# Optimization experiments

Measured on AMD Instinct MI355X. Metric: run time of the kernel, lower is better.

The kernel has to match this reference:

```python
import jax, jax.numpy as jnp
import numpy as np

B, M, D, H, K, V = 4, 2048, 1024, 16, 64, 64

def setup_inputs() -> dict:
    key = jax.random.key(0)
    ks = jax.random.split(key, 5)
    return {
        "x": jax.random.normal(ks[0], (B, M, D), dtype=jnp.float32),
        "P_q": jax.random.normal(ks[1], (H, D, K), dtype=jnp.float32) * 0.02,
        "P_k": jax.random.normal(ks[2], (H, D, K), dtype=jnp.float32) * 0.02,
        "P_v": jax.random.normal(ks[3], (H, D, V), dtype=jnp.float32) * 0.02,
        "P_o": jax.random.normal(ks[4], (H, D, V), dtype=jnp.float32) * 0.02,
    }

def reference(x, P_q, P_k, P_v, P_o):
    # QKV projections: [b,m,d] x [h,d,k] -> [b,h,m,k]
    Q = jnp.einsum('bmd,hdk->bhmk', x, P_q)
    Kt = jnp.einsum('bmd,hdk->bhmk', x, P_k)
    Vt = jnp.einsum('bmd,hdv->bhmv', x, P_v)
    scale = 1.0 / jnp.sqrt(jnp.asarray(K, dtype=x.dtype))
    logits = jnp.einsum('bhmk,bhnk->bhmn', Q, Kt) * scale  # [b,h,m,m]
    m = logits.shape[-1]
    causal = jnp.tril(jnp.ones((m, m), dtype=bool))  # allow j <= i
    logits = jnp.where(causal[None, None], logits, jnp.asarray(-jnp.inf, dtype=logits.dtype))
    weights = jax.nn.softmax(logits, axis=-1)
    o = jnp.einsum('bhmn,bhnv->bhmv', weights, Vt)
    y = jnp.einsum('bhmv,hdv->bmd', o, P_o)
    return y
```

## Files before the change

kernel.cpp:

```cpp
#include <hip/hip_runtime.h>
#include <hip/hip_bf16.h>

#define B_  4
#define M_  2048
#define D_  1024
#define H_  16

typedef __attribute__((ext_vector_type(8)))  short bf16x8;
typedef __attribute__((ext_vector_type(4)))  float f32x4;
typedef __attribute__((ext_vector_type(16))) float f32x16;
typedef __attribute__((ext_vector_type(4)))  unsigned short u16x4;
typedef __attribute__((ext_vector_type(2)))  unsigned int uint2v;

#define MFMA16(a, b, c) __builtin_amdgcn_mfma_f32_16x16x32_bf16((a), (b), (c), 0, 0, 0)
#define MFMA32(a, b, c) __builtin_amdgcn_mfma_f32_32x32x16_bf16((a), (b), (c), 0, 0, 0)

#define QSCALE 0.18033688011112042f

__device__ __forceinline__ unsigned short f2b(float f) {
  union { float f; unsigned u; } v; v.f = f;
  unsigned r = v.u + 0x7FFF + ((v.u >> 16) & 1);
  return (unsigned short)(r >> 16);
}

__device__ __forceinline__ unsigned cvtpk(float lo, float hi) {
  unsigned r;
  asm("v_cvt_pk_bf16_f32 %0, %1, %2" : "=v"(r) : "v"(lo), "v"(hi));
  return r;
}

__device__ __forceinline__ int swzb(int byte) {
  return byte ^ (((byte >> 7) & 7) << 4);
}

#define SWZ256(L) ((L) ^ ((((L) >> 8) & 15) << 4))

#define GLOAD16(gsrc, ldst)                                                     \
  __builtin_amdgcn_global_load_lds(                                             \
      (const __attribute__((address_space(1))) void*)(gsrc),                    \
      (__attribute__((address_space(3))) void*)(ldst), 16, 0, 0)

__global__ __launch_bounds__(256) void convert_x_kernel(
    const float* __restrict__ x, short* __restrict__ xb) {
  const size_t i = ((size_t)blockIdx.x * 256 + threadIdx.x) * 8;
  float4 a = *(const float4*)(x + i);
  float4 b = *(const float4*)(x + i + 4);
  bf16x8 o;
  o[0] = (short)f2b(a.x); o[1] = (short)f2b(a.y); o[2] = (short)f2b(a.z); o[3] = (short)f2b(a.w);
  o[4] = (short)f2b(b.x); o[5] = (short)f2b(b.y); o[6] = (short)f2b(b.z); o[7] = (short)f2b(b.w);
  *(bf16x8*)(xb + i) = o;
}

__global__ __launch_bounds__(256) void convert_w_kernel(
    const float* __restrict__ Pq, const float* __restrict__ Pk,
    const float* __restrict__ Pv, short* __restrict__ Wt) {
  const int idx = blockIdx.x * 256 + threadIdx.x;
  const int n = idx >> 8, d0 = (idx & 255) * 4;
  const int which = n >> 10, h = (n >> 6) & 15, kc = n & 63;
  const float* P = (which == 0) ? Pq : (which == 1) ? Pk : Pv;
  const float* p = P + ((size_t)h * D_ + d0) * 64 + kc;
  u16x4 o;
  o[0] = f2b(p[0]); o[1] = f2b(p[64]); o[2] = f2b(p[128]); o[3] = f2b(p[192]);
  *(u16x4*)(Wt + (size_t)n * D_ + d0) = o;
}

__global__ __launch_bounds__(256) void convert_wo_kernel(
    const float* __restrict__ Po, short* __restrict__ Wo) {
  const int idx = blockIdx.x * 256 + threadIdx.x;
  const int d = idx >> 8, hv0 = (idx & 255) * 4;
  const int h = hv0 >> 6, v = hv0 & 63;
  float4 a = *(const float4*)(Po + ((size_t)h * D_ + d) * 64 + v);
  u16x4 o;
  o[0] = f2b(a.x); o[1] = f2b(a.y); o[2] = f2b(a.z); o[3] = f2b(a.w);
  *(u16x4*)(Wo + (size_t)d * 1024 + hv0) = o;
}

__device__ __forceinline__ void gemm_body_sb(
    const char* __restrict__ Agc, const char* __restrict__ Bgc,
    short* As, short* Bs, int t, int w, int lane,
    f32x4 (&acc)[4][4])
{
  const int wr = (w >> 1) * 64, wc = (w & 1) * 64;
  const int lrow = lane & 15, lgrp = lane >> 4;

  for (int kt = 0; kt < 16; ++kt) {
    __syncthreads();
    const int d2 = kt * 128;
#pragma unroll
    for (int i = 0; i < 4; ++i) {
      const int L = i * 4096 + t * 16;
      const int row = L >> 7;
      const int cs = (L & 127) ^ ((row & 7) << 4);
      GLOAD16(Agc + (size_t)row * 2048 + d2 + cs, (char*)As + L);
      GLOAD16(Bgc + (size_t)row * 2048 + d2 + cs, (char*)Bs + L);
    }
    __syncthreads();
#pragma unroll
    for (int ks = 0; ks < 2; ++ks) {
      bf16x8 a[4], b[4];
      const int cb = ks * 64 + lgrp * 16;
#pragma unroll
      for (int f = 0; f < 4; ++f) {
        a[f] = *(const bf16x8*)((const char*)As + swzb((wr + f * 16 + lrow) * 128 + cb));
        b[f] = *(const bf16x8*)((const char*)Bs + swzb((wc + f * 16 + lrow) * 128 + cb));
      }
      __builtin_amdgcn_s_setprio(1);
#pragma unroll
      for (int mf = 0; mf < 4; ++mf)
#pragma unroll
        for (int nf = 0; nf < 4; ++nf)
          acc[mf][nf] = MFMA16(a[mf], b[nf], acc[mf][nf]);
      __builtin_amdgcn_s_setprio(0);
    }
  }
}

__global__ __launch_bounds__(256) void qkv_gemm_kernel(
    const short* __restrict__ xb, const short* __restrict__ Wt,
    short* __restrict__ Qw, short* __restrict__ Kw, short* __restrict__ Vt) {
  __shared__ short As[8192];
  __shared__ short Bs[8192];
  const int bid = blockIdx.x;
  const int xcd = bid & 7, slot = bid >> 3;
  const int m0 = (xcd * 8 + (slot & 7)) * 128;
  const int n0 = (slot >> 3) * 128;
  const int t = threadIdx.x, lane = t & 63, w = t >> 6;

  f32x4 acc[4][4] = {};
  gemm_body_sb((const char*)xb + (size_t)m0 * 2048,
               (const char*)Wt + (size_t)n0 * 2048,
               As, Bs, t, w, lane, acc);

  const int wr = (w >> 1) * 64, wc = (w & 1) * 64;
  const int lrow = lane & 15, lgrp = lane >> 4;
#pragma unroll
  for (int nf = 0; nf < 4; ++nf) {
    const int n = n0 + wc + nf * 16 + lrow;
    const int which = n >> 10, h = (n >> 6) & 15, kc = n & 63;
#pragma unroll
    for (int mf = 0; mf < 4; ++mf) {
      const int row0 = m0 + wr + mf * 16 + lgrp * 4;
      const int b = row0 >> 11, mm = row0 & 2047;
      const int bh = b * 16 + h;
      if (which == 2) {
        u16x4 o;
        o[0] = f2b(acc[mf][nf][0]); o[1] = f2b(acc[mf][nf][1]);
        o[2] = f2b(acc[mf][nf][2]); o[3] = f2b(acc[mf][nf][3]);
        *(u16x4*)(Vt + ((size_t)bh * 64 + kc) * M_ + mm) = o;
      } else {
        short* outp = (which == 0 ? Qw : Kw) + ((size_t)bh * M_ + mm) * 64 + kc;
        const float scale = (which == 0) ? QSCALE : 1.0f;
#pragma unroll
        for (int r = 0; r < 4; ++r)
          outp[(size_t)r * 64] = (short)f2b(acc[mf][nf][r] * scale);
      }
    }
  }
}

__global__ __launch_bounds__(256) void out_gemm_kernel(
    const short* __restrict__ O2, const short* __restrict__ Wo,
    float* __restrict__ y) {
  __shared__ short As[8192];
  __shared__ short Bs[8192];
  const int bid = blockIdx.x;
  const int xcd = bid & 7, slot = bid >> 3;
  const int m0 = (xcd * 8 + (slot & 7)) * 128;
  const int n0 = (slot >> 3) * 128;
  const int t = threadIdx.x, lane = t & 63, w = t >> 6;

  f32x4 acc[4][4] = {};
  gemm_body_sb((const char*)O2 + (size_t)m0 * 2048,
               (const char*)Wo + (size_t)n0 * 2048,
               As, Bs, t, w, lane, acc);

  const int wr = (w >> 1) * 64, wc = (w & 1) * 64;
  const int lrow = lane & 15, lgrp = lane >> 4;
#pragma unroll
  for (int mf = 0; mf < 4; ++mf)
#pragma unroll
    for (int nf = 0; nf < 4; ++nf) {
      const int n = n0 + wc + nf * 16 + lrow;
      const int row0 = m0 + wr + mf * 16 + lgrp * 4;
#pragma unroll
      for (int r = 0; r < 4; ++r)
        y[(size_t)(row0 + r) * 1024 + n] = acc[mf][nf][r];
    }
}

__device__ __forceinline__ void softmax_chunk(
    f32x16& s0, f32x16& s1, f32x16& o0, f32x16& o1,
    float& mrun, float& lrun, bf16x8 (&pf)[4])
{
  float tm[16];
#pragma unroll
  for (int r = 0; r < 16; ++r) tm[r] = fmaxf(s0[r], s1[r]);
#pragma unroll
  for (int st = 8; st > 0; st >>= 1)
#pragma unroll
    for (int r = 0; r < 8; ++r)
      if (r < st) tm[r] = fmaxf(tm[r], tm[r + st]);
  uint2v pm = __builtin_amdgcn_permlane32_swap(
      __float_as_uint(tm[0]), __float_as_uint(tm[0]), false, false);
  const float mtile = fmaxf(__uint_as_float(pm[0]), __uint_as_float(pm[1]));

  if (!__all(mtile <= mrun + 8.0f)) {
    const float mnew = fmaxf(mrun, mtile);
    const float alpha = __builtin_amdgcn_exp2f(mrun - mnew);
    mrun = mnew;
    lrun *= alpha;
    o0 *= alpha;
    o1 *= alpha;
  }
#pragma unroll
  for (int r = 0; r < 16; ++r) {
    s0[r] = __builtin_amdgcn_exp2f(s0[r] - mrun);
    s1[r] = __builtin_amdgcn_exp2f(s1[r] - mrun);
  }
#pragma unroll
  for (int c = 0; c < 4; ++c) {
    const f32x16& sv = (c < 2) ? s0 : s1;
    const int rb = (c & 1) * 8;
    unsigned a0 = cvtpk(sv[rb + 0], sv[rb + 1]);
    unsigned a1 = cvtpk(sv[rb + 2], sv[rb + 3]);
    unsigned b0 = cvtpk(sv[rb + 4], sv[rb + 5]);
    unsigned b1 = cvtpk(sv[rb + 6], sv[rb + 7]);
    uint2v t0 = __builtin_amdgcn_permlane32_swap(a0, b0, false, false);
    uint2v t1 = __builtin_amdgcn_permlane32_swap(a1, b1, false, false);
    union { unsigned u[4]; bf16x8 v; } pk;
    pk.u[0] = t0[0]; pk.u[1] = t1[0]; pk.u[2] = t0[1]; pk.u[3] = t1[1];
    pf[c] = pk.v;
  }
}

__global__ __launch_bounds__(256) void attn_kernel(
    const short* __restrict__ Qw, const short* __restrict__ Kw,
    const short* __restrict__ Vt, short* __restrict__ O2) {
  __shared__ short Ks[2][64 * 64];
  __shared__ short Vs[2][64 * 64];

  const int bid = blockIdx.x;
  const int chunk = 15 - (bid >> 6);
  const int bh = bid & 63;
  const int q0 = chunk * 128;

  const int t = threadIdx.x, lane = t & 63, w = t >> 6;
  const int l31 = lane & 31, hi = lane >> 5;
  const int qw0 = q0 + w * 32;
  const int qabs = qw0 + l31;

  bf16x8 qfrag[4];
#pragma unroll
  for (int kc = 0; kc < 4; ++kc)
    qfrag[kc] = *(const bf16x8*)(Qw + ((size_t)bh * M_ + qabs) * 64 + kc * 16 + hi * 8);

  f32x16 o0 = {}, o1 = {};
  float mrun = -3.0e38f, lrun = 0.f;

  const char* Kg = (const char*)Kw + (size_t)bh * M_ * 128;
  const char* Vg = (const char*)Vt + (size_t)bh * 64 * M_ * 2;

  auto stage = [&](int bi, int j0_) {
#pragma unroll
    for (int i = 0; i < 2; ++i) {
      const int L  = i * 4096 + t * 16;
      const int Ls = SWZ256(L);
      const int row = Ls >> 7, col = Ls & 127;
      GLOAD16(Kg + (size_t)(j0_ + row) * 128 + col, (char*)Ks[bi] + i * 4096 + w * 1024);
      GLOAD16(Vg + (size_t)row * (M_ * 2) + (size_t)j0_ * 2 + col, (char*)Vs[bi] + i * 4096 + w * 1024);
    }
  };

  const int nt = (q0 + 128) >> 6;
  stage(0, 0);

  bf16x8 ones;
#pragma unroll
  for (int e = 0; e < 8; ++e) ones[e] = (short)0x3F80;

  for (int tt = 0; tt < nt; ++tt) {
    const int j0 = tt << 6;
    const int cur = tt & 1;
    __builtin_amdgcn_s_barrier();
    if (tt + 1 < nt) {
      stage(cur ^ 1, j0 + 64);
      asm volatile("s_waitcnt vmcnt(4)" ::: "memory");
    } else {
      asm volatile("s_waitcnt vmcnt(0)" ::: "memory");
    }
    __builtin_amdgcn_s_barrier();
    if (j0 >= qw0 + 32) continue;

    const char* Kc = (const char*)Ks[cur];
    const char* Vc = (const char*)Vs[cur];

    f32x16 s0 = {}, s1 = {};
    __builtin_amdgcn_s_setprio(1);
#pragma unroll
    for (int kc = 0; kc < 4; ++kc) {
      bf16x8 kf0 = *(const bf16x8*)(Kc + SWZ256(l31 * 128 + kc * 32 + hi * 16));
      s0 = MFMA32(kf0, qfrag[kc], s0);
      bf16x8 kf1 = *(const bf16x8*)(Kc + SWZ256((32 + l31) * 128 + kc * 32 + hi * 16));
      s1 = MFMA32(kf1, qfrag[kc], s1);
    }
    __builtin_amdgcn_s_setprio(0);

    if (j0 + 64 > qw0) {
#pragma unroll
      for (int r = 0; r < 16; ++r) {
        const int k0 = j0 + (r & 3) + 8 * (r >> 2) + 4 * hi;
        if (k0 > qabs)      s0[r] = -3.0e38f;
        if (k0 + 32 > qabs) s1[r] = -3.0e38f;
      }
    }

    bf16x8 pf[4];
    softmax_chunk(s0, s1, o0, o1, mrun, lrun, pf);

    f32x16 lacc = {};
    __builtin_amdgcn_s_setprio(1);
#pragma unroll
    for (int c = 0; c < 4; ++c) {
      bf16x8 vf0 = *(const bf16x8*)(Vc + SWZ256(l31 * 128 + c * 32 + hi * 16));
      o0 = MFMA32(vf0, pf[c], o0);
      bf16x8 vf1 = *(const bf16x8*)(Vc + SWZ256((32 + l31) * 128 + c * 32 + hi * 16));
      o1 = MFMA32(vf1, pf[c], o1);
      lacc = MFMA32(ones, pf[c], lacc);
    }
    __builtin_amdgcn_s_setprio(0);
    lrun += lacc[0];
  }

  const int b = bh >> 4, h = bh & 15;
  const float inv = 1.0f / lrun;
  short* orow = O2 + ((size_t)b * M_ + qabs) * 1024 + h * 64;
#pragma unroll
  for (int vb = 0; vb < 2; ++vb) {
    const f32x16& o = vb ? o1 : o0;
#pragma unroll
    for (int g = 0; g < 4; ++g) {
      const int vbase = vb * 32 + 8 * g + 4 * hi;
      u16x4 pkt;
      pkt[0] = f2b(o[g * 4 + 0] * inv);
      pkt[1] = f2b(o[g * 4 + 1] * inv);
      pkt[2] = f2b(o[g * 4 + 2] * inv);
      pkt[3] = f2b(o[g * 4 + 3] * inv);
      *(u16x4*)(orow + vbase) = pkt;
    }
  }
}

extern "C" void kernel_launch(void* const* d_in, const int* in_sizes, int n_in,
                              void* d_out, int out_size, void* d_ws, size_t ws_size,
                              hipStream_t stream) {
  const float* x  = (const float*)d_in[0];
  const float* Pq = (const float*)d_in[1];
  const float* Pk = (const float*)d_in[2];
  const float* Pv = (const float*)d_in[3];
  const float* Po = (const float*)d_in[4];
  float* y = (float*)d_out;

  short* ws = (short*)d_ws;
  const size_t NX = (size_t)B_ * M_ * D_;
  short* xb  = ws;                 ws += NX;
  short* Wt  = ws;                 ws += (size_t)3072 * 1024;
  short* Wo  = ws;                 ws += (size_t)1024 * 1024;
  short* Qw  = ws;                 ws += NX;
  short* Kw  = ws;                 ws += NX;
  short* Vt  = ws;                 ws += NX;
  short* O2  = ws;                 ws += NX;

  convert_x_kernel <<<4096, 256, 0, stream>>>(x, xb);
  convert_w_kernel <<<3072, 256, 0, stream>>>(Pq, Pk, Pv, Wt);
  convert_wo_kernel<<<1024, 256, 0, stream>>>(Po, Wo);
  qkv_gemm_kernel  <<<1536, 256, 0, stream>>>(xb, Wt, Qw, Kw, Vt);
  attn_kernel      <<<1024, 256, 0, stream>>>(Qw, Kw, Vt, O2);
  out_gemm_kernel  <<<512,  256, 0, stream>>>(O2, Wo, y);
}
```

Before: 179.1 us.

## Merge convert kernels, single-buffer attention LDS, add occupancy hint, flatten max reduction

Combines the three fp32-to-bf16 conversion kernels into one launch that branches on block index, removing two kernel launches. In the attention kernel it drops the double-buffered K/V staging for a single buffer loaded synchronously with two barriers per tile. It also adds a launch-bounds occupancy hint of 6 and rewrites the row-max reduction as a flat fmax tree. The single buffer halves LDS use so more blocks can be resident, but global-load latency is no longer hidden behind compute.

```diff
diff --git a/kernel.cpp b/kernel.cpp
--- a/kernel.cpp
+++ b/kernel.cpp
@@ -40,39 +40,38 @@
       (const __attribute__((address_space(1))) void*)(gsrc),                    \
       (__attribute__((address_space(3))) void*)(ldst), 16, 0, 0)
 
-__global__ __launch_bounds__(256) void convert_x_kernel(
-    const float* __restrict__ x, short* __restrict__ xb) {
-  const size_t i = ((size_t)blockIdx.x * 256 + threadIdx.x) * 8;
-  float4 a = *(const float4*)(x + i);
-  float4 b = *(const float4*)(x + i + 4);
-  bf16x8 o;
-  o[0] = (short)f2b(a.x); o[1] = (short)f2b(a.y); o[2] = (short)f2b(a.z); o[3] = (short)f2b(a.w);
-  o[4] = (short)f2b(b.x); o[5] = (short)f2b(b.y); o[6] = (short)f2b(b.z); o[7] = (short)f2b(b.w);
-  *(bf16x8*)(xb + i) = o;
-}
-
-__global__ __launch_bounds__(256) void convert_w_kernel(
-    const float* __restrict__ Pq, const float* __restrict__ Pk,
-    const float* __restrict__ Pv, short* __restrict__ Wt) {
-  const int idx = blockIdx.x * 256 + threadIdx.x;
-  const int n = idx >> 8, d0 = (idx & 255) * 4;
-  const int which = n >> 10, h = (n >> 6) & 15, kc = n & 63;
-  const float* P = (which == 0) ? Pq : (which == 1) ? Pk : Pv;
-  const float* p = P + ((size_t)h * D_ + d0) * 64 + kc;
-  u16x4 o;
-  o[0] = f2b(p[0]); o[1] = f2b(p[64]); o[2] = f2b(p[128]); o[3] = f2b(p[192]);
-  *(u16x4*)(Wt + (size_t)n * D_ + d0) = o;
-}
-
-__global__ __launch_bounds__(256) void convert_wo_kernel(
-    const float* __restrict__ Po, short* __restrict__ Wo) {
-  const int idx = blockIdx.x * 256 + threadIdx.x;
-  const int d = idx >> 8, hv0 = (idx & 255) * 4;
-  const int h = hv0 >> 6, v = hv0 & 63;
-  float4 a = *(const float4*)(Po + ((size_t)h * D_ + d) * 64 + v);
-  u16x4 o;
-  o[0] = f2b(a.x); o[1] = f2b(a.y); o[2] = f2b(a.z); o[3] = f2b(a.w);
-  *(u16x4*)(Wo + (size_t)d * 1024 + hv0) = o;
+__global__ __launch_bounds__(256) void convert_all_kernel(
+    const float* __restrict__ x,  const float* __restrict__ Pq,
+    const float* __restrict__ Pk, const float* __restrict__ Pv,
+    const float* __restrict__ Po,
+    short* __restrict__ xb, short* __restrict__ Wt, short* __restrict__ Wo) {
+  const int bid = blockIdx.x;
+  if (bid < 4096) {
+    const size_t i = ((size_t)bid * 256 + threadIdx.x) * 8;
+    float4 a = *(const float4*)(x + i);
+    float4 b = *(const float4*)(x + i + 4);
+    bf16x8 o;
+    o[0] = (short)f2b(a.x); o[1] = (short)f2b(a.y); o[2] = (short)f2b(a.z); o[3] = (short)f2b(a.w);
+    o[4] = (short)f2b(b.x); o[5] = (short)f2b(b.y); o[6] = (short)f2b(b.z); o[7] = (short)f2b(b.w);
+    *(bf16x8*)(xb + i) = o;
+  } else if (bid < 7168) {
+    const int idx = (bid - 4096) * 256 + threadIdx.x;
+    const int n = idx >> 8, d0 = (idx & 255) * 4;
+    const int which = n >> 10, h = (n >> 6) & 15, kc = n & 63;
+    const float* P = (which == 0) ? Pq : (which == 1) ? Pk : Pv;
+    const float* p = P + ((size_t)h * D_ + d0) * 64 + kc;
+    u16x4 o;
+    o[0] = f2b(p[0]); o[1] = f2b(p[64]); o[2] = f2b(p[128]); o[3] = f2b(p[192]);
+    *(u16x4*)(Wt + (size_t)n * D_ + d0) = o;
+  } else {
+    const int idx = (bid - 7168) * 256 + threadIdx.x;
+    const int d = idx >> 8, hv0 = (idx & 255) * 4;
+    const int h = hv0 >> 6, v = hv0 & 63;
+    float4 a = *(const float4*)(Po + ((size_t)h * D_ + d) * 64 + v);
+    u16x4 o;
+    o[0] = f2b(a.x); o[1] = f2b(a.y); o[2] = f2b(a.z); o[3] = f2b(a.w);
+    *(u16x4*)(Wo + (size_t)d * 1024 + hv0) = o;
+  }
 }
 
 __device__ __forceinline__ void gemm_body_sb(
@@ -192,16 +191,16 @@
     f32x16& s0, f32x16& s1, f32x16& o0, f32x16& o1,
     float& mrun, float& lrun, bf16x8 (&pf)[4])
 {
-  float tm[16];
-#pragma unroll
-  for (int r = 0; r < 16; ++r) tm[r] = fmaxf(s0[r], s1[r]);
-#pragma unroll
-  for (int st = 8; st > 0; st >>= 1)
-#pragma unroll
-    for (int r = 0; r < 8; ++r)
-      if (r < st) tm[r] = fmaxf(tm[r], tm[r + st]);
+  float a[8];
+#pragma unroll
+  for (int r = 0; r < 8; ++r)
+    a[r] = fmaxf(fmaxf(fmaxf(s0[r], s0[r + 8]), s1[r]), s1[r + 8]);
+  float b0 = fmaxf(fmaxf(a[0], a[1]), a[2]);
+  float b1 = fmaxf(fmaxf(a[3], a[4]), a[5]);
+  float b2 = fmaxf(fmaxf(a[6], a[7]), b0);
+  float tmax = fmaxf(b1, b2);
   uint2v pm = __builtin_amdgcn_permlane32_swap(
-      __float_as_uint(tm[0]), __float_as_uint(tm[0]), false, false);
+      __float_as_uint(tmax), __float_as_uint(tmax), false, false);
   const float mtile = fmaxf(__uint_as_float(pm[0]), __uint_as_float(pm[1]));
 
   if (!__all(mtile <= mrun + 8.0f)) {
@@ -223,21 +222,21 @@
     const int rb = (c & 1) * 8;
     unsigned a0 = cvtpk(sv[rb + 0], sv[rb + 1]);
     unsigned a1 = cvtpk(sv[rb + 2], sv[rb + 3]);
-    unsigned b0 = cvtpk(sv[rb + 4], sv[rb + 5]);
-    unsigned b1 = cvtpk(sv[rb + 6], sv[rb + 7]);
-    uint2v t0 = __builtin_amdgcn_permlane32_swap(a0, b0, false, false);
-    uint2v t1 = __builtin_amdgcn_permlane32_swap(a1, b1, false, false);
+    unsigned b0_ = cvtpk(sv[rb + 4], sv[rb + 5]);
+    unsigned b1_ = cvtpk(sv[rb + 6], sv[rb + 7]);
+    uint2v t0 = __builtin_amdgcn_permlane32_swap(a0, b0_, false, false);
+    uint2v t1 = __builtin_amdgcn_permlane32_swap(a1, b1_, false, false);
     union { unsigned u[4]; bf16x8 v; } pk;
     pk.u[0] = t0[0]; pk.u[1] = t1[0]; pk.u[2] = t0[1]; pk.u[3] = t1[1];
     pf[c] = pk.v;
   }
 }
 
-__global__ __launch_bounds__(256) void attn_kernel(
+__global__ __launch_bounds__(256, 6) void attn_kernel(
     const short* __restrict__ Qw, const short* __restrict__ Kw,
     const short* __restrict__ Vt, short* __restrict__ O2) {
-  __shared__ short Ks[2][64 * 64];
-  __shared__ short Vs[2][64 * 64];
+  __shared__ short Ks[64 * 64];
+  __shared__ short Vs[64 * 64];
 
   const int bid = blockIdx.x;
   const int chunk = 15 - (bid >> 6);
@@ -260,19 +259,18 @@
   const char* Kg = (const char*)Kw + (size_t)bh * M_ * 128;
   const char* Vg = (const char*)Vt + (size_t)bh * 64 * M_ * 2;
 
-  auto stage = [&](int bi, int j0_) {
+  auto stage = [&](int j0_) {
 #pragma unroll
     for (int i = 0; i < 2; ++i) {
       const int L  = i * 4096 + t * 16;
       const int Ls = SWZ256(L);
       const int row = Ls >> 7, col = Ls & 127;
-      GLOAD16(Kg + (size_t)(j0_ + row) * 128 + col, (char*)Ks[bi] + i * 4096 + w * 1024);
-      GLOAD16(Vg + (size_t)row * (M_ * 2) + (size_t)j0_ * 2 + col, (char*)Vs[bi] + i * 4096 + w * 1024);
+      GLOAD16(Kg + (size_t)(j0_ + row) * 128 + col, (char*)Ks + i * 4096 + w * 1024);
+      GLOAD16(Vg + (size_t)row * (M_ * 2) + (size_t)j0_ * 2 + col, (char*)Vs + i * 4096 + w * 1024);
     }
   };
 
   const int nt = (q0 + 128) >> 6;
-  stage(0, 0);
 
   bf16x8 ones;
 #pragma unroll
@@ -280,27 +278,18 @@
 
   for (int tt = 0; tt < nt; ++tt) {
     const int j0 = tt << 6;
-    const int cur = tt & 1;
-    __builtin_amdgcn_s_barrier();
-    if (tt + 1 < nt) {
-      stage(cur ^ 1, j0 + 64);
-      asm volatile("s_waitcnt vmcnt(4)" ::: "memory");
-    } else {
-      asm volatile("s_waitcnt vmcnt(0)" ::: "memory");
-    }
-    __builtin_amdgcn_s_barrier();
+    __syncthreads();
+    stage(j0);
+    __syncthreads();
     if (j0 >= qw0 + 32) continue;
-
-    const char* Kc = (const char*)Ks[cur];
-    const char* Vc = (const char*)Vs[cur];
 
     f32x16 s0 = {}, s1 = {};
     __builtin_amdgcn_s_setprio(1);
 #pragma unroll
     for (int kc = 0; kc < 4; ++kc) {
-      bf16x8 kf0 = *(const bf16x8*)(Kc + SWZ256(l31 * 128 + kc * 32 + hi * 16));
+      bf16x8 kf0 = *(const bf16x8*)((const char*)Ks + SWZ256(l31 * 128 + kc * 32 + hi * 16));
       s0 = MFMA32(kf0, qfrag[kc], s0);
-      bf16x8 kf1 = *(const bf16x8*)(Kc + SWZ256((32 + l31) * 128 + kc * 32 + hi * 16));
+      bf16x8 kf1 = *(const bf16x8*)((const char*)Ks + SWZ256((32 + l31) * 128 + kc * 32 + hi * 16));
       s1 = MFMA32(kf1, qfrag[kc], s1);
     }
     __builtin_amdgcn_s_setprio(0);
@@ -321,9 +310,9 @@
     __builtin_amdgcn_s_setprio(1);
 #pragma unroll
     for (int c = 0; c < 4; ++c) {
-      bf16x8 vf0 = *(const bf16x8*)(Vc + SWZ256(l31 * 128 + c * 32 + hi * 16));
+      bf16x8 vf0 = *(const bf16x8*)((const char*)Vs + SWZ256(l31 * 128 + c * 32 + hi * 16));
       o0 = MFMA32(vf0, pf[c], o0);
-      bf16x8 vf1 = *(const bf16x8*)(Vc + SWZ256((32 + l31) * 128 + c * 32 + hi * 16));
+      bf16x8 vf1 = *(const bf16x8*)((const char*)Vs + SWZ256((32 + l31) * 128 + c * 32 + hi * 16));
       o1 = MFMA32(vf1, pf[c], o1);
       lacc = MFMA32(ones, pf[c], lacc);
     }
@@ -370,10 +359,8 @@
   short* Vt  = ws;                 ws += NX;
   short* O2  = ws;                 ws += NX;
 
-  convert_x_kernel <<<4096, 256, 0, stream>>>(x, xb);
-  convert_w_kernel <<<3072, 256, 0, stream>>>(Pq, Pk, Pv, Wt);
-  convert_wo_kernel<<<1024, 256, 0, stream>>>(Po, Wo);
-  qkv_gemm_kernel  <<<1536, 256, 0, stream>>>(xb, Wt, Qw, Kw, Vt);
-  attn_kernel      <<<1024, 256, 0, stream>>>(Qw, Kw, Vt, O2);
-  out_gemm_kernel  <<<512,  256, 0, stream>>>(O2, Wo, y);
-}
+  convert_all_kernel<<<8192, 256, 0, stream>>>(x, Pq, Pk, Pv, Po, xb, Wt, Wo);
+  qkv_gemm_kernel   <<<1536, 256, 0, stream>>>(xb, Wt, Qw, Kw, Vt);
+  attn_kernel       <<<1024, 256, 0, stream>>>(Qw, Kw, Vt, O2);
+  out_gemm_kernel   <<<512,  256, 0, stream>>>(O2, Wo, y);
+}
```

Result: slower. 245.9 us (+37.3%).
